# Performance work log

Hardware: AMD Instinct MI355X
Metric: run time of the kernel (lower is better)

The kernel has to match this reference:

```python
import jax, jax.numpy as jnp
import numpy as np

N = 50000
E = 800000
IN_C, HID, OUT_C = 128, 128, 64
EPS = 1e-5


def gcn_conv(x, edge_index, W, b):
    # x: [N, F_in], edge_index: [2, E], W: [F_in, F_out], b: [F_out]
    src, dst = edge_index[0], edge_index[1]
    h = x @ W  # [N, F_out]
    # degree with self-loops (edge weight 1)
    deg = 1.0 + jax.ops.segment_sum(jnp.ones((E,), h.dtype), dst, num_segments=N)
    dinv = jax.lax.rsqrt(deg)  # deg^{-1/2}
    coef = dinv[src] * dinv[dst]  # [E]
    msg = h[src] * coef[:, None]  # gather + scale
    agg = jax.ops.segment_sum(msg, dst, num_segments=N)
    agg = agg + h * (dinv * dinv)[:, None]  # self-loop term deg^{-1}
    return agg + b


def bn_eval(x, gamma, beta, mean, var):
    return (x - mean) * jax.lax.rsqrt(var + EPS) * gamma + beta


def leaky(x):
    return jnp.where(x > 0, x, 0.1 * x)


def setup_inputs() -> dict:
    key = jax.random.key(0)
    ks = jax.random.split(key, 12)
    x = jax.random.normal(ks[0], (N, IN_C), jnp.float32)
    edge_index = jax.random.randint(ks[1], (2, E), 0, N, dtype=jnp.int64)
    s1 = 1.0 / np.sqrt(IN_C)
    s2 = 1.0 / np.sqrt(HID)
    W1 = jax.random.uniform(ks[2], (IN_C, HID), jnp.float32, -s1, s1)
    b1 = jnp.zeros((HID,), jnp.float32)
    W2 = jax.random.uniform(ks[3], (HID, HID), jnp.float32, -s2, s2)
    b2 = jnp.zeros((HID,), jnp.float32)
    W3 = jax.random.uniform(ks[4], (HID, OUT_C), jnp.float32, -s2, s2)
    b3 = jnp.zeros((OUT_C,), jnp.float32)
    g1 = jnp.ones((HID,), jnp.float32)
    be1 = jnp.zeros((HID,), jnp.float32)
    m1 = 0.1 * jax.random.normal(ks[5], (HID,), jnp.float32)
    v1 = jax.random.uniform(ks[6], (HID,), jnp.float32, 0.5, 1.5)
    g2 = jnp.ones((HID,), jnp.float32)
    be2 = jnp.zeros((HID,), jnp.float32)
    m2 = 0.1 * jax.random.normal(ks[7], (HID,), jnp.float32)
    v2 = jax.random.uniform(ks[8], (HID,), jnp.float32, 0.5, 1.5)
    return dict(x=x, edge_index=edge_index, W1=W1, b1=b1, g1=g1, be1=be1, m1=m1, v1=v1,
                W2=W2, b2=b2, g2=g2, be2=be2, m2=m2, v2=v2, W3=W3, b3=b3)


def reference(x, edge_index, W1, b1, g1, be1, m1, v1, W2, b2, g2, be2, m2, v2, W3, b3):
    h = gcn_conv(x, edge_index, W1, b1)
    h = leaky(bn_eval(h, g1, be1, m1, v1))
    # dropout is identity at inference
    h = gcn_conv(h, edge_index, W2, b2)
    h = leaky(bn_eval(h, g2, be2, m2, v2))
    z = gcn_conv(h, edge_index, W3, b3)
    return z
```

## Files before the change

kernel.cpp:

```cpp
#include <hip/hip_runtime.h>
#include <hip/hip_fp16.h>


#define LRELU_SLOPE 0.1f
#define BN_EPS 1e-5f
#define BCAP 20480

typedef _Float16 half8 __attribute__((ext_vector_type(8)));
typedef float f32x4 __attribute__((ext_vector_type(4)));

__global__ void prep_all(const float* __restrict__ W1, const float* __restrict__ W2,
                         const float* __restrict__ W3, _Float16* __restrict__ W1t,
                         _Float16* __restrict__ W2t, _Float16* __restrict__ W3t,
                         const float* __restrict__ b1, const float* __restrict__ g1,
                         const float* __restrict__ be1, const float* __restrict__ m1,
                         const float* __restrict__ v1,
                         const float* __restrict__ b2, const float* __restrict__ g2,
                         const float* __restrict__ be2, const float* __restrict__ m2,
                         const float* __restrict__ v2,
                         const float* __restrict__ b3,
                         float* __restrict__ sc1, float* __restrict__ sh1,
                         float* __restrict__ sc2, float* __restrict__ sh2,
                         float* __restrict__ sc3, float* __restrict__ sh3,
                         int* __restrict__ bcur) {
    int i = blockIdx.x * 256 + threadIdx.x;
    if (i < 16384) {
        int k = i >> 7, c = i & 127;
        W1t[c * 136 + k] = (_Float16)W1[i];
    } else if (i < 32768) {
        int j = i - 16384;
        int k = j >> 7, c = j & 127;
        W2t[c * 136 + k] = (_Float16)W2[j];
    } else if (i < 40960) {
        int j = i - 32768;
        int k = j >> 6, c = j & 63;
        W3t[c * 136 + k] = (_Float16)W3[j];
    } else if (i < 41088) {
        int f = i - 40960;
        float s = g1[f] * rsqrtf(v1[f] + BN_EPS);
        sc1[f] = s;
        sh1[f] = (b1[f] - m1[f]) * s + be1[f];
    } else if (i < 41216) {
        int f = i - 41088;
        float s = g2[f] * rsqrtf(v2[f] + BN_EPS);
        sc2[f] = s;
        sh2[f] = (b2[f] - m2[f]) * s + be2[f];
    } else if (i < 41280) {
        int f = i - 41216;
        sc3[f] = 1.0f;
        sh3[f] = b3[f];
    } else if (i < 41344) {
        bcur[i - 41280] = (i - 41280) * BCAP;
    }
}

__global__ __launch_bounds__(256) void bin_pass(const int* __restrict__ src,
                                                const int* __restrict__ dst, int E,
                                                int* __restrict__ bcur,
                                                unsigned long long* __restrict__ pairs) {
    __shared__ int sd[1664], ss[1664];
    __shared__ int lcur[64];
    const int tid = threadIdx.x;
    const int chunk = (E + gridDim.x - 1) / gridDim.x;
    const int e0 = blockIdx.x * chunk;
    const int ecnt = min(chunk, E - e0);
    for (int j = tid; j < ecnt; j += 256) {
        sd[j] = dst[e0 + j];
        ss[j] = src[e0 + j];
    }
    if (tid < 64) lcur[tid] = 0;
    __syncthreads();
    for (int j = tid; j < ecnt; j += 256) atomicAdd(&lcur[sd[j] >> 10], 1);
    __syncthreads();
    if (tid < 64) lcur[tid] = atomicAdd(&bcur[tid], lcur[tid]);
    __syncthreads();
    for (int j = tid; j < ecnt; j += 256) {
        const int b = sd[j] >> 10;
        const int pos = atomicAdd(&lcur[b], 1);
        pairs[pos] = ((unsigned long long)(unsigned)ss[j] << 32) | (unsigned)sd[j];
    }
}

__global__ __launch_bounds__(512) void hist_bucket(const unsigned long long* __restrict__ pairs,
                                                   const int* __restrict__ bcur,
                                                   int* __restrict__ cnt, int N) {
    __shared__ int h[1024];
    const int b = blockIdx.x;
    const int base = b << 10;
    const int nn = min(1024, N - base);
    const int cntb = bcur[b] - b * BCAP;
    for (int i = threadIdx.x; i < 1024; i += 512) h[i] = 0;
    __syncthreads();
    const unsigned long long* pb = pairs + (size_t)b * BCAP;
    for (int j = threadIdx.x; j < cntb; j += 512) {
        const int d = (int)(pb[j] & 0xffffffffull);
        atomicAdd(&h[d - base], 1);
    }
    __syncthreads();
    for (int i = threadIdx.x; i < nn; i += 512) cnt[base + i] = h[i];
}

__global__ void scan1(const int* __restrict__ cnt, int* __restrict__ incl,
                      int* __restrict__ part, int n) {
    __shared__ int s[256];
    int tid = threadIdx.x;
    int gid = blockIdx.x * 256 + tid;
    int v = (gid < n) ? cnt[gid] : 0;
    s[tid] = v;
    __syncthreads();
    for (int off = 1; off < 256; off <<= 1) {
        int t = (tid >= off) ? s[tid - off] : 0;
        __syncthreads();
        s[tid] += t;
        __syncthreads();
    }
    if (gid < n) incl[gid] = s[tid];
    if (tid == 255) part[blockIdx.x] = s[255];
}

__global__ void scan23(const int* __restrict__ cnt, const int* __restrict__ incl,
                       const int* __restrict__ part, int* __restrict__ row_ptr,
                       float* __restrict__ dinv, int n, int E) {
    __shared__ int red[256];
    const int tid = threadIdx.x;
    int acc = 0;
    for (int i = tid; i < blockIdx.x; i += 256) acc += part[i];
    red[tid] = acc;
    __syncthreads();
    for (int off = 128; off > 0; off >>= 1) {
        if (tid < off) red[tid] += red[tid + off];
        __syncthreads();
    }
    const int pof = red[0];
    const int gid = blockIdx.x * 256 + tid;
    if (gid < n) {
        int c = cnt[gid];
        row_ptr[gid] = incl[gid] - c + pof;
        dinv[gid] = rsqrtf(1.0f + (float)c);
    }
    if (gid == 0) row_ptr[n] = E;
}

__global__ __launch_bounds__(512) void build_csr(const unsigned long long* __restrict__ pairs,
                                                 const int* __restrict__ bcur,
                                                 const int* __restrict__ row_ptr,
                                                 int* __restrict__ ssrc_g, int N) {
    __shared__ int cur[1024];
    const int b = blockIdx.x;
    const int base = b << 10;
    const int nn = min(1024, N - base);
    const int cntb = bcur[b] - b * BCAP;
    for (int i = threadIdx.x; i < nn; i += 512) cur[i] = row_ptr[base + i];
    __syncthreads();
    const unsigned long long* pb = pairs + (size_t)b * BCAP;
    for (int j = threadIdx.x; j < cntb; j += 512) {
        const unsigned long long p = pb[j];
        const int d = (int)(p & 0xffffffffull);
        const int s = (int)(p >> 32);
        const int pos = atomicAdd(&cur[d - base], 1);
        ssrc_g[pos] = s;
    }
}

template <int NC, bool AF32>
__global__ __launch_bounds__(256) void gemm_mfma(const void* __restrict__ Ain,
                                                 const _Float16* __restrict__ Wt,
                                                 const float* __restrict__ dinv,
                                                 __half* __restrict__ H, int nrows) {
    constexpr int NT = NC / 16;
    constexpr int SPH = (NC == 128) ? 136 : 88;
    __shared__ _Float16 smem[NC * 136];

    const int tid = threadIdx.x;
    const int row0 = blockIdx.x * 64;

    {
        const uint4* src = reinterpret_cast<const uint4*>(Wt);
        uint4* dst = reinterpret_cast<uint4*>(smem);
        for (int i = tid; i < NC * 17; i += 256) dst[i] = src[i];
    }
    __syncthreads();

    const int w = tid >> 6;
    const int lane = tid & 63;
    const int l15 = lane & 15;
    const int kg = lane >> 4;

    int ar = row0 + w * 16 + l15;
    if (ar > nrows - 1) ar = nrows - 1;
    half8 a[4];
#pragma unroll
    for (int ks = 0; ks < 4; ++ks) {
        const int cb = ks * 32 + kg * 8;
        if constexpr (AF32) {
            const float* Xf = (const float*)Ain;
            const float4 x0 = *reinterpret_cast<const float4*>(&Xf[(size_t)ar * 128 + cb]);
            const float4 x1 = *reinterpret_cast<const float4*>(&Xf[(size_t)ar * 128 + cb + 4]);
            half8 av;
            av[0] = (_Float16)x0.x; av[1] = (_Float16)x0.y;
            av[2] = (_Float16)x0.z; av[3] = (_Float16)x0.w;
            av[4] = (_Float16)x1.x; av[5] = (_Float16)x1.y;
            av[6] = (_Float16)x1.z; av[7] = (_Float16)x1.w;
            a[ks] = av;
        } else {
            const __half* Xh = (const __half*)Ain;
            a[ks] = *reinterpret_cast<const half8*>(&Xh[(size_t)ar * 128 + cb]);
        }
    }

    f32x4 acc[NT];
#pragma unroll
    for (int nt = 0; nt < NT; ++nt) acc[nt] = {0.f, 0.f, 0.f, 0.f};

#pragma unroll
    for (int nt = 0; nt < NT; ++nt) {
        const int c = nt * 16 + l15;
#pragma unroll
        for (int ks = 0; ks < 4; ++ks) {
            const half8 b = *reinterpret_cast<const half8*>(&smem[c * 136 + ks * 32 + kg * 8]);
            acc[nt] = __builtin_amdgcn_mfma_f32_16x16x32_f16(a[ks], b, acc[nt], 0, 0, 0);
        }
    }

    __syncthreads();

    float dv[4];
#pragma unroll
    for (int r = 0; r < 4; ++r) {
        int gr = row0 + w * 16 + kg * 4 + r;
        if (gr > nrows - 1) gr = nrows - 1;
        dv[r] = dinv[gr];
    }
    _Float16* Hl = smem;
#pragma unroll
    for (int nt = 0; nt < NT; ++nt) {
#pragma unroll
        for (int r = 0; r < 4; ++r) {
            Hl[(w * 16 + kg * 4 + r) * SPH + nt * 16 + l15] = (_Float16)(acc[nt][r] * dv[r]);
        }
    }
    __syncthreads();

    constexpr int CG = NC / 8;
    for (int i = tid; i < 64 * CG; i += 256) {
        const int row = i / CG, cg = i % CG;
        const int gr = row0 + row;
        if (gr < nrows) {
            *reinterpret_cast<uint4*>(&H[(size_t)gr * NC + cg * 8]) =
                *reinterpret_cast<const uint4*>(&Hl[row * SPH + cg * 8]);
        }
    }
}

__device__ __forceinline__ float2 u2f2(unsigned u) {
    __half2 h;
    *reinterpret_cast<unsigned*>(&h) = u;
    return __half22float2(h);
}

template <int NC, bool ACT, bool HOUT>
__global__ __launch_bounds__(256) void agg_h(
    const __half* __restrict__ H, const int* __restrict__ row_ptr,
    const int* __restrict__ ssrc, const float* __restrict__ dinv,
    const float* __restrict__ sc, const float* __restrict__ sh,
    void* __restrict__ out, int n) {
    constexpr int FPT = NC / 32;
    const int tid = threadIdx.x;
    const int node = blockIdx.x * 8 + (tid >> 5);
    const int lane = tid & 31;
    const int f0 = lane * FPT;
    if (node >= n) return;

    const int e0 = row_ptr[node];
    const int e1 = row_ptr[node + 1];

    if constexpr (FPT == 4) {
        uint2 su = *reinterpret_cast<const uint2*>(&H[(size_t)node * NC + f0]);
        float2 slo = u2f2(su.x), shi = u2f2(su.y);
        float4 A0 = {slo.x, slo.y, shi.x, shi.y};
        float4 A1 = {0, 0, 0, 0}, A2 = {0, 0, 0, 0}, A3 = {0, 0, 0, 0};
        int e = e0;
        for (; e + 7 < e1; e += 8) {
            int s[8];
#pragma unroll
            for (int j = 0; j < 8; ++j) s[j] = ssrc[e + j];
            uint2 u[8];
#pragma unroll
            for (int j = 0; j < 8; ++j)
                u[j] = *reinterpret_cast<const uint2*>(&H[(size_t)s[j] * NC + f0]);
#pragma unroll
            for (int j = 0; j < 8; ++j) {
                float2 l = u2f2(u[j].x), h = u2f2(u[j].y);
                float4& A = (j & 3) == 0 ? A0 : (j & 3) == 1 ? A1 : (j & 3) == 2 ? A2 : A3;
                A.x += l.x; A.y += l.y; A.z += h.x; A.w += h.y;
            }
        }
        for (; e < e1; ++e) {
            const uint2 u = *reinterpret_cast<const uint2*>(&H[(size_t)ssrc[e] * NC + f0]);
            float2 l = u2f2(u.x), h = u2f2(u.y);
            A1.x += l.x; A1.y += l.y; A1.z += h.x; A1.w += h.y;
        }
        float4 acc;
        acc.x = (A0.x + A1.x) + (A2.x + A3.x);
        acc.y = (A0.y + A1.y) + (A2.y + A3.y);
        acc.z = (A0.z + A1.z) + (A2.z + A3.z);
        acc.w = (A0.w + A1.w) + (A2.w + A3.w);
        const float dn = dinv[node];
        const float4 scv = *reinterpret_cast<const float4*>(&sc[f0]);
        const float4 shv = *reinterpret_cast<const float4*>(&sh[f0]);
        float o[4];
        o[0] = fmaf(acc.x * dn, scv.x, shv.x);
        o[1] = fmaf(acc.y * dn, scv.y, shv.y);
        o[2] = fmaf(acc.z * dn, scv.z, shv.z);
        o[3] = fmaf(acc.w * dn, scv.w, shv.w);
        if constexpr (ACT) {
#pragma unroll
            for (int j = 0; j < 4; ++j) o[j] = o[j] > 0.f ? o[j] : LRELU_SLOPE * o[j];
        }
        if constexpr (HOUT) {
            __half2 p0 = __floats2half2_rn(o[0], o[1]);
            __half2 p1 = __floats2half2_rn(o[2], o[3]);
            uint2 st;
            st.x = *reinterpret_cast<unsigned*>(&p0);
            st.y = *reinterpret_cast<unsigned*>(&p1);
            *reinterpret_cast<uint2*>(&((__half*)out)[(size_t)node * NC + f0]) = st;
        } else {
            float4 ov = {o[0], o[1], o[2], o[3]};
            *reinterpret_cast<float4*>(&((float*)out)[(size_t)node * NC + f0]) = ov;
        }
    } else {
        unsigned su = *reinterpret_cast<const unsigned*>(&H[(size_t)node * NC + f0]);
        float2 A0 = u2f2(su);
        float2 A1 = {0, 0}, A2 = {0, 0}, A3 = {0, 0};
        int e = e0;
        for (; e + 7 < e1; e += 8) {
            int s[8];
#pragma unroll
            for (int j = 0; j < 8; ++j) s[j] = ssrc[e + j];
            unsigned u[8];
#pragma unroll
            for (int j = 0; j < 8; ++j)
                u[j] = *reinterpret_cast<const unsigned*>(&H[(size_t)s[j] * NC + f0]);
#pragma unroll
            for (int j = 0; j < 8; ++j) {
                float2 f = u2f2(u[j]);
                float2& A = (j & 3) == 0 ? A0 : (j & 3) == 1 ? A1 : (j & 3) == 2 ? A2 : A3;
                A.x += f.x; A.y += f.y;
            }
        }
        for (; e < e1; ++e) {
            float2 f = u2f2(*reinterpret_cast<const unsigned*>(&H[(size_t)ssrc[e] * NC + f0]));
            A1.x += f.x; A1.y += f.y;
        }
        float2 acc;
        acc.x = (A0.x + A1.x) + (A2.x + A3.x);
        acc.y = (A0.y + A1.y) + (A2.y + A3.y);
        const float dn = dinv[node];
        const float2 scv = *reinterpret_cast<const float2*>(&sc[f0]);
        const float2 shv = *reinterpret_cast<const float2*>(&sh[f0]);
        float o0 = fmaf(acc.x * dn, scv.x, shv.x);
        float o1 = fmaf(acc.y * dn, scv.y, shv.y);
        if constexpr (ACT) {
            o0 = o0 > 0.f ? o0 : LRELU_SLOPE * o0;
            o1 = o1 > 0.f ? o1 : LRELU_SLOPE * o1;
        }
        if constexpr (HOUT) {
            __half2 p0 = __floats2half2_rn(o0, o1);
            *reinterpret_cast<unsigned*>(&((__half*)out)[(size_t)node * NC + f0]) =
                *reinterpret_cast<unsigned*>(&p0);
        } else {
            float2 ov = {o0, o1};
            *reinterpret_cast<float2*>(&((float*)out)[(size_t)node * NC + f0]) = ov;
        }
    }
}

extern "C" void kernel_launch(void* const* d_in, const int* in_sizes, int n_in,
                              void* d_out, int out_size, void* d_ws, size_t ws_size,
                              hipStream_t stream) {
    const float* x  = (const float*)d_in[0];
    const int* ei   = (const int*)d_in[1];
    const float* W1 = (const float*)d_in[2];
    const float* b1 = (const float*)d_in[3];
    const float* g1 = (const float*)d_in[4];
    const float* be1= (const float*)d_in[5];
    const float* m1 = (const float*)d_in[6];
    const float* v1 = (const float*)d_in[7];
    const float* W2 = (const float*)d_in[8];
    const float* b2 = (const float*)d_in[9];
    const float* g2 = (const float*)d_in[10];
    const float* be2= (const float*)d_in[11];
    const float* m2 = (const float*)d_in[12];
    const float* v2 = (const float*)d_in[13];
    const float* W3 = (const float*)d_in[14];
    const float* b3 = (const float*)d_in[15];
    float* out = (float*)d_out;

    const int N = in_sizes[0] / 128;
    const int E = in_sizes[1] / 2;
    const int* srcIdx = ei;
    const int* dstIdx = ei + E;
    const int nbuck = (N + 1023) >> 10;

    char* p = (char*)d_ws;
    auto carve = [&](size_t bytes) -> void* {
        void* r = (void*)p;
        p += (bytes + 255) & ~(size_t)255;
        return r;
    };
    int* cnt       = (int*)carve((size_t)N * 4);
    int* incl      = (int*)carve((size_t)N * 4);
    int* part      = (int*)carve(1024);
    int* row_ptr   = (int*)carve((size_t)(N + 1) * 4);
    int* bcur      = (int*)carve(64 * 4);
    float* dinv    = (float*)carve((size_t)N * 4);
    int* ssrc      = (int*)carve((size_t)E * 4);
    unsigned long long* pairs = (unsigned long long*)carve((size_t)nbuck * BCAP * 8);
    __half* Hb     = (__half*)carve((size_t)N * 128 * 2);
    __half* Xb     = (__half*)carve((size_t)N * 128 * 2);
    _Float16* W1t  = (_Float16*)carve(128 * 136 * 2);
    _Float16* W2t  = (_Float16*)carve(128 * 136 * 2);
    _Float16* W3t  = (_Float16*)carve(64 * 136 * 2);
    float* sc1     = (float*)carve(128 * 4);
    float* sh1     = (float*)carve(128 * 4);
    float* sc2     = (float*)carve(128 * 4);
    float* sh2     = (float*)carve(128 * 4);
    float* sc3     = (float*)carve(64 * 4);
    float* sh3     = (float*)carve(64 * 4);
    (void)ws_size; (void)n_in; (void)out_size;

    const int nb_n = (N + 255) / 256;

    prep_all<<<162, 256, 0, stream>>>(W1, W2, W3, W1t, W2t, W3t,
                                      b1, g1, be1, m1, v1, b2, g2, be2, m2, v2, b3,
                                      sc1, sh1, sc2, sh2, sc3, sh3, bcur);
    bin_pass<<<512, 256, 0, stream>>>(srcIdx, dstIdx, E, bcur, pairs);
    hist_bucket<<<nbuck, 512, 0, stream>>>(pairs, bcur, cnt, N);
    scan1<<<nb_n, 256, 0, stream>>>(cnt, incl, part, N);
    scan23<<<nb_n, 256, 0, stream>>>(cnt, incl, part, row_ptr, dinv, N, E);
    build_csr<<<nbuck, 512, 0, stream>>>(pairs, bcur, row_ptr, ssrc, N);

    const int gb = (N + 63) / 64;
    const int ab = (N + 7) / 8;

    gemm_mfma<128, true><<<gb, 256, 0, stream>>>(x, W1t, dinv, Hb, N);
    agg_h<128, true, true><<<ab, 256, 0, stream>>>(
        Hb, row_ptr, ssrc, dinv, sc1, sh1, Xb, N);

    gemm_mfma<128, false><<<gb, 256, 0, stream>>>(Xb, W2t, dinv, Hb, N);
    agg_h<128, true, true><<<ab, 256, 0, stream>>>(
        Hb, row_ptr, ssrc, dinv, sc2, sh2, Xb, N);

    gemm_mfma<64, false><<<gb, 256, 0, stream>>>(Xb, W3t, dinv, Hb, N);
    agg_h<64, false, false><<<ab, 256, 0, stream>>>(
        Hb, row_ptr, ssrc, dinv, sc3, sh3, out, N);
}
```

Before: 269.7 us.

## Fuse histogram and scan into per-bucket kernels and pack edge pairs into 32 bits

Edge pairs are packed as src<<10 | local dst into 32-bit words instead of 64-bit, halving traffic on the bucket buffer. The per-bucket histogram now also does the 1024-wide exclusive scan in shared memory and computes dinv. Cross-bucket offsets are applied in the CSR scatter kernel via a wavefront reduction. This replaces four kernels with two, removing launches and intermediate count arrays. The packing assumes src fits in 22 bits and at most 64 buckets.

```diff
diff --git a/kernel.cpp b/kernel.cpp
--- a/kernel.cpp
+++ b/kernel.cpp
@@ -57,7 +57,7 @@
 __global__ __launch_bounds__(256) void bin_pass(const int* __restrict__ src,
                                                 const int* __restrict__ dst, int E,
                                                 int* __restrict__ bcur,
-                                                unsigned long long* __restrict__ pairs) {
+                                                unsigned* __restrict__ pairs) {
     __shared__ int sd[1664], ss[1664];
     __shared__ int lcur[64];
     const int tid = threadIdx.x;
@@ -75,90 +75,78 @@
     if (tid < 64) lcur[tid] = atomicAdd(&bcur[tid], lcur[tid]);
     __syncthreads();
     for (int j = tid; j < ecnt; j += 256) {
-        const int b = sd[j] >> 10;
-        const int pos = atomicAdd(&lcur[b], 1);
-        pairs[pos] = ((unsigned long long)(unsigned)ss[j] << 32) | (unsigned)sd[j];
-    }
-}
-
-__global__ __launch_bounds__(512) void hist_bucket(const unsigned long long* __restrict__ pairs,
-                                                   const int* __restrict__ bcur,
-                                                   int* __restrict__ cnt, int N) {
+        const int d = sd[j];
+        const int pos = atomicAdd(&lcur[d >> 10], 1);
+        pairs[pos] = ((unsigned)ss[j] << 10) | (unsigned)(d & 1023);
+    }
+}
+
+__global__ __launch_bounds__(1024) void hist_scan(const unsigned* __restrict__ pairs,
+                                                  const int* __restrict__ bcur,
+                                                  int* __restrict__ row_ptr,
+                                                  float* __restrict__ dinv,
+                                                  int* __restrict__ part, int N) {
     __shared__ int h[1024];
+    __shared__ int s[1024];
     const int b = blockIdx.x;
+    const int tid = threadIdx.x;
     const int base = b << 10;
     const int nn = min(1024, N - base);
     const int cntb = bcur[b] - b * BCAP;
-    for (int i = threadIdx.x; i < 1024; i += 512) h[i] = 0;
-    __syncthreads();
-    const unsigned long long* pb = pairs + (size_t)b * BCAP;
-    for (int j = threadIdx.x; j < cntb; j += 512) {
-        const int d = (int)(pb[j] & 0xffffffffull);
-        atomicAdd(&h[d - base], 1);
-    }
-    __syncthreads();
-    for (int i = threadIdx.x; i < nn; i += 512) cnt[base + i] = h[i];
-}
-
-__global__ void scan1(const int* __restrict__ cnt, int* __restrict__ incl,
-                      int* __restrict__ part, int n) {
-    __shared__ int s[256];
-    int tid = threadIdx.x;
-    int gid = blockIdx.x * 256 + tid;
-    int v = (gid < n) ? cnt[gid] : 0;
+    h[tid] = 0;
+    __syncthreads();
+    const unsigned* pb = pairs + (size_t)b * BCAP;
+    for (int j = tid; j < cntb; j += 1024) atomicAdd(&h[pb[j] & 1023u], 1);
+    __syncthreads();
+    const int v = h[tid];
     s[tid] = v;
     __syncthreads();
-    for (int off = 1; off < 256; off <<= 1) {
+    for (int off = 1; off < 1024; off <<= 1) {
         int t = (tid >= off) ? s[tid - off] : 0;
         __syncthreads();
         s[tid] += t;
         __syncthreads();
     }
-    if (gid < n) incl[gid] = s[tid];
-    if (tid == 255) part[blockIdx.x] = s[255];
-}
-
-__global__ void scan23(const int* __restrict__ cnt, const int* __restrict__ incl,
-                       const int* __restrict__ part, int* __restrict__ row_ptr,
-                       float* __restrict__ dinv, int n, int E) {
-    __shared__ int red[256];
+    if (tid < nn) {
+        row_ptr[base + tid] = s[tid] - v;
+        dinv[base + tid] = rsqrtf(1.0f + (float)v);
+    }
+    if (tid == 1023) part[b] = s[1023];
+}
+
+__global__ __launch_bounds__(1024) void csr_scatter(const unsigned* __restrict__ pairs,
+                                                    const int* __restrict__ bcur,
+                                                    const int* __restrict__ part,
+                                                    int* __restrict__ row_ptr,
+                                                    int* __restrict__ ssrc_g,
+                                                    int N, int E, int nbuck) {
+    __shared__ int cur[1024];
+    __shared__ int pofs;
+    const int b = blockIdx.x;
     const int tid = threadIdx.x;
-    int acc = 0;
-    for (int i = tid; i < blockIdx.x; i += 256) acc += part[i];
-    red[tid] = acc;
-    __syncthreads();
-    for (int off = 128; off > 0; off >>= 1) {
-        if (tid < off) red[tid] += red[tid + off];
-        __syncthreads();
-    }
-    const int pof = red[0];
-    const int gid = blockIdx.x * 256 + tid;
-    if (gid < n) {
-        int c = cnt[gid];
-        row_ptr[gid] = incl[gid] - c + pof;
-        dinv[gid] = rsqrtf(1.0f + (float)c);
-    }
-    if (gid == 0) row_ptr[n] = E;
-}
-
-__global__ __launch_bounds__(512) void build_csr(const unsigned long long* __restrict__ pairs,
-                                                 const int* __restrict__ bcur,
-                                                 const int* __restrict__ row_ptr,
-                                                 int* __restrict__ ssrc_g, int N) {
-    __shared__ int cur[1024];
-    const int b = blockIdx.x;
     const int base = b << 10;
     const int nn = min(1024, N - base);
     const int cntb = bcur[b] - b * BCAP;
-    for (int i = threadIdx.x; i < nn; i += 512) cur[i] = row_ptr[base + i];
-    __syncthreads();
-    const unsigned long long* pb = pairs + (size_t)b * BCAP;
-    for (int j = threadIdx.x; j < cntb; j += 512) {
-        const unsigned long long p = pb[j];
-        const int d = (int)(p & 0xffffffffull);
-        const int s = (int)(p >> 32);
-        const int pos = atomicAdd(&cur[d - base], 1);
-        ssrc_g[pos] = s;
+    if (tid < 64) {
+        int v = (tid < b) ? part[tid] : 0;
+#pragma unroll
+        for (int off = 32; off; off >>= 1) v += __shfl_down(v, off, 64);
+        if (tid == 0) pofs = v;
+    }
+    __syncthreads();
+    const int pof = pofs;
+    if (tid < nn) {
+        const int rp = row_ptr[base + tid] + pof;
+        row_ptr[base + tid] = rp;
+        cur[tid] = rp;
+    }
+    if (b == nbuck - 1 && tid == 0) row_ptr[N] = E;
+    __syncthreads();
+    const unsigned* pb = pairs + (size_t)b * BCAP;
+    for (int j = tid; j < cntb; j += 1024) {
+        const unsigned p = pb[j];
+        const int pos = atomicAdd(&cur[p & 1023u], 1);
+        ssrc_g[pos] = (int)(p >> 10);
     }
 }
 
@@ -408,14 +396,12 @@
         p += (bytes + 255) & ~(size_t)255;
         return r;
     };
-    int* cnt       = (int*)carve((size_t)N * 4);
-    int* incl      = (int*)carve((size_t)N * 4);
     int* part      = (int*)carve(1024);
     int* row_ptr   = (int*)carve((size_t)(N + 1) * 4);
     int* bcur      = (int*)carve(64 * 4);
     float* dinv    = (float*)carve((size_t)N * 4);
     int* ssrc      = (int*)carve((size_t)E * 4);
-    unsigned long long* pairs = (unsigned long long*)carve((size_t)nbuck * BCAP * 8);
+    unsigned* pairs = (unsigned*)carve((size_t)nbuck * BCAP * 4);
     __half* Hb     = (__half*)carve((size_t)N * 128 * 2);
     __half* Xb     = (__half*)carve((size_t)N * 128 * 2);
     _Float16* W1t  = (_Float16*)carve(128 * 136 * 2);
@@ -429,16 +415,12 @@
     float* sh3     = (float*)carve(64 * 4);
     (void)ws_size; (void)n_in; (void)out_size;
 
-    const int nb_n = (N + 255) / 256;
-
     prep_all<<<162, 256, 0, stream>>>(W1, W2, W3, W1t, W2t, W3t,
                                       b1, g1, be1, m1, v1, b2, g2, be2, m2, v2, b3,
                                       sc1, sh1, sc2, sh2, sc3, sh3, bcur);
     bin_pass<<<512, 256, 0, stream>>>(srcIdx, dstIdx, E, bcur, pairs);
-    hist_bucket<<<nbuck, 512, 0, stream>>>(pairs, bcur, cnt, N);
-    scan1<<<nb_n, 256, 0, stream>>>(cnt, incl, part, N);
-    scan23<<<nb_n, 256, 0, stream>>>(cnt, incl, part, row_ptr, dinv, N, E);
-    build_csr<<<nbuck, 512, 0, stream>>>(pairs, bcur, row_ptr, ssrc, N);
+    hist_scan<<<nbuck, 1024, 0, stream>>>(pairs, bcur, row_ptr, dinv, part, N);
+    csr_scatter<<<nbuck, 1024, 0, stream>>>(pairs, bcur, part, row_ptr, ssrc, N, E, nbuck);
 
     const int gb = (N + 63) / 64;
     const int ab = (N + 7) / 8;
```

Result: faster. 261.8 us (-3.0%).
